# Performance work log

Hardware: AMD Instinct MI355X
Metric: run time of the kernel (lower is better)

Reference implementation:

```python
import jax, jax.numpy as jnp
import numpy as np

B, L, H = 2, 2048, 1024
NH, DK, DV = 4, 256, 256
CONV_K, FIR_S, FIR_L = 4, 3, 63
GATE_IN = H + 4 * 2 * NH  # 1056
MLP_H = 2 * H
CHUNK = 32


def l2norm(x):
    return x * jax.lax.rsqrt(jnp.sum(x * x, -1, keepdims=True) + 1e-6)


def causal_dwconv(x, w):
    # x: [b, l, c], w: [c, k]; causal depthwise cross-correlation == F.conv1d(pad left k-1, groups=c)
    k = w.shape[-1]
    xc = jnp.pad(jnp.transpose(x, (0, 2, 1)), ((0, 0), (0, 0), (k - 1, 0)))
    y = jax.lax.conv_general_dilated(xc, w[:, None, :], (1,), 'VALID',
                                     feature_group_count=w.shape[0],
                                     dimension_numbers=('NCH', 'OIH', 'NCH'))
    return jnp.transpose(y, (0, 2, 1))


def delta_rule_chunkwise(q, k, v, beta, chunk=CHUNK):
    # q,k: [b,h,L,dk]; v: [b,h,L,dv]; beta: [b,h,L]; L divisible by chunk
    b, h, Lp, dk = q.shape
    dv = v.shape[-1]
    n = Lp // chunk
    q = l2norm(q)
    k = l2norm(k)
    v = v * beta[..., None]
    kb = k * beta[..., None]
    qc, kc, vc, kbc = (t.reshape(b, h, n, chunk, -1) for t in (q, k, v, kb))
    # strictly-lower Gram matrix; the original in-place row loop computes inv(I + tril(kb k^T, -1))
    A = jnp.tril(jnp.einsum('bhnid,bhnjd->bhnij', kbc, kc), -1)
    T = jnp.linalg.inv(jnp.eye(chunk, dtype=q.dtype) + A)  # [b,h,n,c,c]
    u = T @ vc   # [b,h,n,c,dv]
    w = T @ kbc  # [b,h,n,c,dk]

    def step(S, inp):
        qi, ki, ui, wi = inp  # each [b,h,c,d]
        attn = jnp.tril(qi @ jnp.swapaxes(ki, -1, -2))  # keep diag (masked_fill triu(.,1))
        u2 = ui - wi @ S
        oi = qi @ S + attn @ u2
        return S + jnp.swapaxes(ki, -1, -2) @ u2, oi

    S0 = jnp.zeros((b, h, dk, dv), q.dtype)
    xs = tuple(jnp.moveaxis(t, 2, 0) for t in (qc, kc, u, w))
    S, o = jax.lax.scan(step, S0, xs)
    o = jnp.moveaxis(o, 0, 2).reshape(b, h, Lp, dv)
    return o, S


def branch_stats(x):
    # x: [b,l,h,d] -> [b,l,2h]  (mean and population-std, std clamped at sqrt(1e-6))
    m = x.mean(-1)
    s = jnp.sqrt(jnp.maximum(x.var(-1), 1e-6))
    return jnp.concatenate([m, s], -1)


def setup_inputs() -> dict:
    key = jax.random.key(0)
    ks = jax.random.split(key, 16)
    f32 = jnp.float32

    def dirac(k_, shape):
        f = 0.01 * jax.random.normal(k_, shape, f32)
        return f.at[..., shape[-1] // 2].add(1.0)

    b2 = jnp.zeros((NH * 4,), f32).at[jnp.arange(NH) * 4 + 3].set(2.0)
    return {
        'hidden_states': jax.random.normal(ks[0], (B, L, H), f32),
        'Wq': 0.02 * jax.random.normal(ks[1], (H, NH * DK), f32),
        'Wk': 0.02 * jax.random.normal(ks[2], (H, NH * DK), f32),
        'Wv': 0.02 * jax.random.normal(ks[3], (H, NH * DV), f32),
        'Wb': 0.02 * jax.random.normal(ks[4], (H, NH), f32),
        'conv_q_w': 0.2 * jax.random.normal(ks[5], (NH * DK, CONV_K), f32),
        'conv_k_w': 0.2 * jax.random.normal(ks[6], (NH * DK, CONV_K), f32),
        'conv_v_w': 0.2 * jax.random.normal(ks[7], (NH * DV, CONV_K), f32),
        'fir_short_w': dirac(ks[8], (NH, DV, FIR_S)),
        'fir_long_w': dirac(ks[9], (NH, DV, FIR_L)),
        'mlp_w1': 0.02 * jax.random.normal(ks[10], (GATE_IN, MLP_H), f32),
        'mlp_b1': jnp.zeros((MLP_H,), f32),
        'mlp_w2': 0.02 * jax.random.normal(ks[11], (MLP_H, NH * 4), f32),
        'mlp_b2': b2,
        'gate_log_temp': jnp.full((NH,), np.log(1.2), f32),
        'o_norm_w': jnp.ones((DV,), f32),
        'Wo': 0.02 * jax.random.normal(ks[12], (NH * DV, H), f32),
    }


def reference(hidden_states, Wq, Wk, Wv, Wb, conv_q_w, conv_k_w, conv_v_w,
              fir_short_w, fir_long_w, mlp_w1, mlp_b1, mlp_w2, mlp_b2,
              gate_log_temp, o_norm_w, Wo):
    x = hidden_states
    b, l, _ = x.shape
    # projections + short causal depthwise convs with silu (qk_activation='silu')
    q = jax.nn.silu(causal_dwconv(x @ Wq, conv_q_w)).reshape(b, l, NH, DK)
    k = jax.nn.silu(causal_dwconv(x @ Wk, conv_k_w)).reshape(b, l, NH, DK)
    v = jax.nn.silu(causal_dwconv(x @ Wv, conv_v_w)).reshape(b, l, NH, DV)
    beta = jax.nn.sigmoid(x @ Wb)  # [b,l,h]

    delta_out, _S = delta_rule_chunkwise(
        jnp.transpose(q, (0, 2, 1, 3)), jnp.transpose(k, (0, 2, 1, 3)),
        jnp.transpose(v, (0, 2, 1, 3)), jnp.transpose(beta, (0, 2, 1)))
    delta_out = jnp.transpose(delta_out, (0, 2, 1, 3))  # [b,l,h,dv]

    vf = v.reshape(b, l, NH * DV)
    fir_short = causal_dwconv(vf, fir_short_w.reshape(NH * DV, FIR_S)).reshape(b, l, NH, DV)
    fir_long = causal_dwconv(vf, fir_long_w.reshape(NH * DV, FIR_L)).reshape(b, l, NH, DV)

    gate_in = jnp.concatenate([x, branch_stats(fir_short), branch_stats(fir_long),
                               branch_stats(delta_out), branch_stats(v)], -1)
    logits = jax.nn.gelu(gate_in @ mlp_w1 + mlp_b1, approximate=False) @ mlp_w2 + mlp_b2
    temp = jax.nn.softplus(gate_log_temp) + 1e-4
    logits = logits.reshape(b, l, NH, 4) / temp[None, None, :, None]
    w = jax.nn.softmax(logits, -1)

    o = (w[..., 0:1] * fir_short + w[..., 1:2] * fir_long
         + w[..., 2:3] * delta_out + w[..., 3:4] * v)
    # RMSNorm over head_v_dim, eps=1e-5
    o = o * jax.lax.rsqrt(jnp.mean(o * o, -1, keepdims=True) + 1e-5) * o_norm_w
    return o.reshape(b, l, NH * DV) @ Wo
```

## Files before the change

### kernel.cpp

```cpp
#include <hip/hip_runtime.h>
#include <hip/hip_bf16.h>


#define DEVI __device__ __forceinline__
typedef unsigned int u32;
typedef unsigned short ushort_t;
typedef __attribute__((ext_vector_type(8))) short short8;
typedef __attribute__((ext_vector_type(4))) float floatx4;

constexpr int Ls = 2048, NH = 4;

constexpr size_t off_xq   = 0;
constexpr size_t off_xk   = 4194304;
constexpr size_t off_xv   = 8388608;
constexpr size_t off_q    = 12582912;
constexpr size_t off_k    = 16777216;
constexpr size_t off_v    = 20971520;
constexpr size_t off_beta = 25165824;
constexpr size_t off_attn = 25182208;
constexpr size_t off_firs = 25706496;
constexpr size_t off_firl = 29900800;
constexpr size_t off_gin  = 34095104;
constexpr size_t off_mlph = 38420480;
constexpr size_t off_gates= 46809088;

DEVI float sigmoidf_(float x) { return 1.f / (1.f + expf(-x)); }
DEVI float siluf_(float x) { return x / (1.f + expf(-x)); }
DEVI float geluf_(float x) { return 0.5f * x * (1.f + erff(x * 0.7071067811865476f)); }
DEVI ushort_t f2bf(float f) {
  union { float f; u32 u; } c{f};
  u32 r = (c.u + 0x7fffu + ((c.u >> 16) & 1u)) >> 16;
  return (ushort_t)r;
}
DEVI float bf2f(ushort_t h) {
  union { u32 u; float f; } c; c.u = ((u32)h) << 16; return c.f;
}
DEVI void cvt8(float4 a, float4 b, short8& hi, short8& lo) {
  float f[8] = {a.x,a.y,a.z,a.w,b.x,b.y,b.z,b.w};
#pragma unroll
  for (int j = 0; j < 8; ++j) {
    ushort_t h = f2bf(f[j]);
    hi[j] = (short)h;
    lo[j] = (short)f2bf(f[j] - bf2f(h));
  }
}
DEVI void async16(const void* g, void* l) {
  __builtin_amdgcn_global_load_lds(
      (const u32 __attribute__((address_space(1)))*)g,
      (u32 __attribute__((address_space(3)))*)l, 16, 0, 0);
}
DEVI void wave_barrier() {
  __builtin_amdgcn_sched_barrier(0);
  asm volatile("s_waitcnt lgkmcnt(0)" ::: "memory");
  __builtin_amdgcn_s_barrier();
  __builtin_amdgcn_sched_barrier(0);
}

__global__ __launch_bounds__(256) void to_bf16(
    const float* __restrict__ in, ushort_t* __restrict__ out, int n)
{
  int i = (blockIdx.x * 256 + threadIdx.x) * 8;
  if (i >= n) return;
  float4 a = *(const float4*)(in + i);
  float4 b = *(const float4*)(in + i + 4);
  ushort_t o[8] = { f2bf(a.x), f2bf(a.y), f2bf(a.z), f2bf(a.w),
                    f2bf(b.x), f2bf(b.y), f2bf(b.z), f2bf(b.w) };
  *(uint4*)(out + i) = *(uint4*)o;
}

__global__ __launch_bounds__(256) void convT(
    const float* __restrict__ W, ushort_t* __restrict__ out, int Kq, int Nq)
{
  __shared__ ushort_t tile[32][33];
  int n0 = blockIdx.x * 32, k0 = blockIdx.y * 32;
  int tx = threadIdx.x & 31, ty = threadIdx.x >> 5;
#pragma unroll
  for (int r = 0; r < 32; r += 8)
    tile[ty + r][tx] = f2bf(W[(size_t)(k0 + ty + r) * Nq + n0 + tx]);
  __syncthreads();
#pragma unroll
  for (int r = 0; r < 32; r += 8)
    out[(size_t)(n0 + ty + r) * Kq + k0 + tx] = tile[tx][ty + r];
}

__global__ __launch_bounds__(256) void gemm_bf16(
    const ushort_t* __restrict__ A, const ushort_t* __restrict__ Bt,
    float* __restrict__ C, int Nq, int Kq,
    const float* __restrict__ bias, int act, int outbf)
{
  __shared__ ushort_t As[128 * 32];
  __shared__ ushort_t Bs[128 * 32];
  int t = threadIdx.x;
  int w = t >> 6, lane = t & 63;
  int m0 = blockIdx.y * 128, n0 = blockIdx.x * 128;
  floatx4 acc[4][4];
#pragma unroll
  for (int i = 0; i < 4; ++i)
#pragma unroll
    for (int j = 0; j < 4; ++j)
#pragma unroll
      for (int r = 0; r < 4; ++r) acc[i][j][r] = 0.f;

  int lrow = lane >> 2, lk8 = (lane & 3) * 8;
  for (int kt = 0; kt < Kq; kt += 32) {
#pragma unroll
    for (int r = 0; r < 2; ++r) {
      int seg = w * 2 + r;
      int row = seg * 16 + lrow;
      async16(A  + (size_t)(m0 + row) * Kq + kt + lk8, &As[seg * 512]);
      async16(Bt + (size_t)(n0 + row) * Kq + kt + lk8, &Bs[seg * 512]);
    }
    __syncthreads();
    short8 af[4], bf[4];
#pragma unroll
    for (int i = 0; i < 4; ++i) {
      int row = (w >> 1) * 64 + i * 16 + (lane & 15);
      af[i] = *(const short8*)&As[row * 32 + (lane >> 4) * 8];
    }
#pragma unroll
    for (int j = 0; j < 4; ++j) {
      int col = (w & 1) * 64 + j * 16 + (lane & 15);
      bf[j] = *(const short8*)&Bs[col * 32 + (lane >> 4) * 8];
    }
#pragma unroll
    for (int i = 0; i < 4; ++i)
#pragma unroll
      for (int j = 0; j < 4; ++j)
        acc[i][j] = __builtin_amdgcn_mfma_f32_16x16x32_bf16(af[i], bf[j], acc[i][j], 0, 0, 0);
    __syncthreads();
  }
#pragma unroll
  for (int i = 0; i < 4; ++i) {
    int rbase = m0 + (w >> 1) * 64 + i * 16 + ((lane >> 4) << 2);
#pragma unroll
    for (int j = 0; j < 4; ++j) {
      int col = n0 + (w & 1) * 64 + j * 16 + (lane & 15);
      float bv = act ? bias[col] : 0.f;
#pragma unroll
      for (int r = 0; r < 4; ++r) {
        float v = acc[i][j][r];
        if (act) v = geluf_(v + bv);
        if (outbf) ((ushort_t*)C)[(size_t)(rbase + r) * Nq + col] = f2bf(v);
        else       C[(size_t)(rbase + r) * Nq + col] = v;
      }
    }
  }
}

__global__ __launch_bounds__(256) void beta_sigmoid(
    const float* __restrict__ x, const float* __restrict__ Wb,
    float* __restrict__ beta)
{
  int mtok = blockIdx.x, t = threadIdx.x;
  int b = mtok >> 11, l = mtok & 2047;
  float a0 = 0, a1 = 0, a2 = 0, a3 = 0;
  for (int k = t; k < 1024; k += 256) {
    float xv = x[(size_t)mtok * 1024 + k];
    float4 w4 = *(const float4*)(Wb + k * 4);
    a0 = fmaf(xv, w4.x, a0); a1 = fmaf(xv, w4.y, a1);
    a2 = fmaf(xv, w4.z, a2); a3 = fmaf(xv, w4.w, a3);
  }
#pragma unroll
  for (int off = 32; off; off >>= 1) {
    a0 += __shfl_down(a0, off); a1 += __shfl_down(a1, off);
    a2 += __shfl_down(a2, off); a3 += __shfl_down(a3, off);
  }
  __shared__ float red[4][4];
  int w = t >> 6;
  if ((t & 63) == 0) { red[w][0] = a0; red[w][1] = a1; red[w][2] = a2; red[w][3] = a3; }
  __syncthreads();
  if (t < 4) {
    float s = red[0][t] + red[1][t] + red[2][t] + red[3][t];
    beta[((size_t)(b * NH + t)) * Ls + l] = sigmoidf_(s);
  }
}

__global__ __launch_bounds__(256) void conv_prep(
    const float* __restrict__ x3, const float* __restrict__ wq,
    const float* __restrict__ wk, const float* __restrict__ wv,
    const float* __restrict__ beta_g,
    float* __restrict__ qn, float* __restrict__ kn,
    float* __restrict__ kb, float* __restrict__ vb,
    float* __restrict__ v_out)
{
  int i = blockIdx.x;
  int t = threadIdx.x;
  int l = i & 2047, bh = i >> 11;
  int b = bh >> 2, h = bh & 3;
  int c = h * 256 + t;
  const float* p = x3 + ((size_t)b * Ls) * 3072 + c;
  float4 wq4 = *(const float4*)(wq + c * 4);
  float4 wk4 = *(const float4*)(wk + c * 4);
  float4 wv4 = *(const float4*)(wv + c * 4);
  float qw[4] = {wq4.x, wq4.y, wq4.z, wq4.w};
  float kw[4] = {wk4.x, wk4.y, wk4.z, wk4.w};
  float vw[4] = {wv4.x, wv4.y, wv4.z, wv4.w};
  float aq = 0.f, ak = 0.f, av = 0.f;
#pragma unroll
  for (int j = 0; j < 4; ++j) {
    int ls = l - 3 + j;
    if (ls >= 0) {
      size_t rb = (size_t)ls * 3072;
      aq = fmaf(qw[j], p[rb], aq);
      ak = fmaf(kw[j], p[rb + 1024], ak);
      av = fmaf(vw[j], p[rb + 2048], av);
    }
  }
  float qv = siluf_(aq), kv = siluf_(ak), vv = siluf_(av);
  float sq = qv * qv, sk = kv * kv;
#pragma unroll
  for (int off = 32; off; off >>= 1) {
    sq += __shfl_down(sq, off);
    sk += __shfl_down(sk, off);
  }
  __shared__ float rq_[4], rk_[4];
  int w = t >> 6;
  if ((t & 63) == 0) { rq_[w] = sq; rk_[w] = sk; }
  __syncthreads();
  sq = rq_[0] + rq_[1] + rq_[2] + rq_[3];
  sk = rk_[0] + rk_[1] + rk_[2] + rk_[3];
  float rq = rsqrtf(sq + 1e-6f), rk = rsqrtf(sk + 1e-6f);
  float bt = beta_g[i];
  size_t base = (size_t)i * 256 + t;
  qn[base] = qv * rq;
  kn[base] = kv * rk;
  kb[base] = kv * rk * bt;
  vb[base] = vv * bt;
  v_out[base] = vv;
}

__global__ __launch_bounds__(256) void chunk_prep(
    const float* __restrict__ kb, const float* __restrict__ kn,
    const float* __restrict__ qn, const float* __restrict__ vb,
    float* __restrict__ attn_g, float* __restrict__ u_out,
    ushort_t* __restrict__ wn_bf, ushort_t* __restrict__ q_bf,
    ushort_t* __restrict__ knT_bf, ushort_t* __restrict__ kn_bf)
{
  __shared__ float Am[32][33];
  __shared__ float Tm[32][36];
  __shared__ ushort_t KT_hi[256][40];
  __shared__ ushort_t KT_lo[256][40];
  int t = threadIdx.x;
  int cc = blockIdx.x & 63, bh = blockIdx.x >> 6;
  size_t gbase = ((size_t)bh * Ls + cc * 32) * 256;
  int wv = t >> 6, lane = t & 63;
  int l16 = lane & 15, quad = lane >> 4;
  int mi = wv >> 1, ni = wv & 1;

  floatx4 Aacc = {0.f,0.f,0.f,0.f}, Qacc = {0.f,0.f,0.f,0.f};
  {
    int mrow = mi * 16 + l16, nrow = ni * 16 + l16;
    const float* kbp = kb + gbase + (size_t)mrow * 256;
    const float* qnp = qn + gbase + (size_t)mrow * 256;
    const float* knp = kn + gbase + (size_t)nrow * 256;
#pragma unroll
    for (int ks = 0; ks < 8; ++ks) {
      int koff = ks * 32 + quad * 8;
      short8 kbh, kbl, qnh, qnl, knh, knl;
      cvt8(*(const float4*)(kbp + koff), *(const float4*)(kbp + koff + 4), kbh, kbl);
      cvt8(*(const float4*)(qnp + koff), *(const float4*)(qnp + koff + 4), qnh, qnl);
      cvt8(*(const float4*)(knp + koff), *(const float4*)(knp + koff + 4), knh, knl);
      Aacc = __builtin_amdgcn_mfma_f32_16x16x32_bf16(kbh, knh, Aacc, 0, 0, 0);
      Aacc = __builtin_amdgcn_mfma_f32_16x16x32_bf16(kbh, knl, Aacc, 0, 0, 0);
      Aacc = __builtin_amdgcn_mfma_f32_16x16x32_bf16(kbl, knh, Aacc, 0, 0, 0);
      Qacc = __builtin_amdgcn_mfma_f32_16x16x32_bf16(qnh, knh, Qacc, 0, 0, 0);
      Qacc = __builtin_amdgcn_mfma_f32_16x16x32_bf16(qnh, knl, Qacc, 0, 0, 0);
      Qacc = __builtin_amdgcn_mfma_f32_16x16x32_bf16(qnl, knh, Qacc, 0, 0, 0);
      if (ni == 0)
        *(uint4*)(q_bf + gbase + (size_t)mrow * 256 + koff) = *(uint4*)&qnh;
      if (mi == 0)
        *(uint4*)(kn_bf + gbase + (size_t)nrow * 256 + koff) = *(uint4*)&knh;
    }
  }
  float* ag = attn_g + ((size_t)bh * 64 + cc) * 1024;
#pragma unroll
  for (int r = 0; r < 4; ++r) {
    int row = mi * 16 + quad * 4 + r, col = ni * 16 + l16;
    Am[row][col] = (col < row) ? Aacc[r] : 0.f;
    ag[row * 32 + col] = (col <= row) ? Qacc[r] : 0.f;
  }
  __syncthreads();

  if (wv == 0) {
    if (t < 32) {
#pragma unroll
      for (int i = 0; i < 32; ++i) Tm[i][t] = (i == t) ? 1.f : 0.f;
      for (int i2 = 1; i2 < 32; ++i2) {
        if (t < i2) {
          float s = 0.f;
          for (int m2 = t; m2 < i2; ++m2) s = fmaf(Am[i2][m2], Tm[m2][t], s);
          Tm[i2][t] = -s;
        }
      }
    }
  } else {
    int base = t - 64;
#pragma unroll
    for (int pass = 0; pass < 2; ++pass) {
      int d = base + pass * 192;
      if (d < 256) {
        u32 hp[16], lp[16], kp2[16];
#pragma unroll
        for (int m2 = 0; m2 < 16; ++m2) {
          float f0 = kb[gbase + (size_t)(2 * m2) * 256 + d];
          float f1 = kb[gbase + (size_t)(2 * m2 + 1) * 256 + d];
          ushort_t h0 = f2bf(f0), h1 = f2bf(f1);
          hp[m2] = (u32)h0 | ((u32)h1 << 16);
          lp[m2] = (u32)f2bf(f0 - bf2f(h0)) | ((u32)f2bf(f1 - bf2f(h1)) << 16);
          float g0 = kn[gbase + (size_t)(2 * m2) * 256 + d];
          float g1 = kn[gbase + (size_t)(2 * m2 + 1) * 256 + d];
          kp2[m2] = (u32)f2bf(g0) | ((u32)f2bf(g1) << 16);
        }
#pragma unroll
        for (int q2 = 0; q2 < 4; ++q2) {
          *(uint4*)&KT_hi[d][q2 * 8] = *(uint4*)&hp[q2 * 4];
          *(uint4*)&KT_lo[d][q2 * 8] = *(uint4*)&lp[q2 * 4];
          *(uint4*)(knT_bf + gbase + (size_t)d * 32 + q2 * 8) = *(uint4*)&kp2[q2 * 4];
        }
      }
    }
  }
  __syncthreads();

  int lt = wv & 1, dgrp = wv >> 1;
  short8 Th, Tl;
  {
    int lrow = lt * 16 + l16;
    cvt8(*(const float4*)&Tm[lrow][quad * 8],
         *(const float4*)&Tm[lrow][quad * 8 + 4], Th, Tl);
  }
#pragma unroll
  for (int j = 0; j < 8; ++j) {
    int dt = dgrp * 8 + j;
    short8 Bh = *(const short8*)&KT_hi[dt * 16 + l16][quad * 8];
    short8 Bl = *(const short8*)&KT_lo[dt * 16 + l16][quad * 8];
    floatx4 acc = {0.f,0.f,0.f,0.f};
    acc = __builtin_amdgcn_mfma_f32_16x16x32_bf16(Th, Bh, acc, 0, 0, 0);
    acc = __builtin_amdgcn_mfma_f32_16x16x32_bf16(Th, Bl, acc, 0, 0, 0);
    acc = __builtin_amdgcn_mfma_f32_16x16x32_bf16(Tl, Bh, acc, 0, 0, 0);
#pragma unroll
    for (int r = 0; r < 4; ++r) {
      int row = lt * 16 + quad * 4 + r;
      wn_bf[gbase + (size_t)row * 256 + dt * 16 + l16] = f2bf(-acc[r]);
    }
  }
  __syncthreads();

  {
    int d = t;
    u32 hp[16], lp[16];
#pragma unroll
    for (int m2 = 0; m2 < 16; ++m2) {
      float f0 = vb[gbase + (size_t)(2 * m2) * 256 + d];
      float f1 = vb[gbase + (size_t)(2 * m2 + 1) * 256 + d];
      ushort_t h0 = f2bf(f0), h1 = f2bf(f1);
      hp[m2] = (u32)h0 | ((u32)h1 << 16);
      lp[m2] = (u32)f2bf(f0 - bf2f(h0)) | ((u32)f2bf(f1 - bf2f(h1)) << 16);
    }
#pragma unroll
    for (int q2 = 0; q2 < 4; ++q2) {
      *(uint4*)&KT_hi[d][q2 * 8] = *(uint4*)&hp[q2 * 4];
      *(uint4*)&KT_lo[d][q2 * 8] = *(uint4*)&lp[q2 * 4];
    }
  }
  __syncthreads();

#pragma unroll
  for (int j = 0; j < 8; ++j) {
    int dt = dgrp * 8 + j;
    short8 Bh = *(const short8*)&KT_hi[dt * 16 + l16][quad * 8];
    short8 Bl = *(const short8*)&KT_lo[dt * 16 + l16][quad * 8];
    floatx4 acc = {0.f,0.f,0.f,0.f};
    acc = __builtin_amdgcn_mfma_f32_16x16x32_bf16(Th, Bh, acc, 0, 0, 0);
    acc = __builtin_amdgcn_mfma_f32_16x16x32_bf16(Th, Bl, acc, 0, 0, 0);
    acc = __builtin_amdgcn_mfma_f32_16x16x32_bf16(Tl, Bh, acc, 0, 0, 0);
#pragma unroll
    for (int r = 0; r < 4; ++r) {
      int row = lt * 16 + quad * 4 + r;
      u_out[gbase + (size_t)row * 256 + dt * 16 + l16] = acc[r];
    }
  }
}

__global__ __launch_bounds__(256) void cross_prep(
    const ushort_t* __restrict__ wn_bf, const ushort_t* __restrict__ q_bf,
    const ushort_t* __restrict__ kn_bf,
    float* __restrict__ X_g, float* __restrict__ Y_g)
{
  int t = threadIdx.x;
  int sc = blockIdx.x & 31, bh = blockIdx.x >> 5;
  int wv = t >> 6, lane = t & 63;
  int l16 = lane & 15, quad = lane >> 4;
  int mi = wv >> 1, ni = wv & 1;
  size_t base = (size_t)bh * Ls * 256;
  size_t r1 = base + (size_t)(sc * 64 + 32 + mi * 16 + l16) * 256;
  size_t r0 = base + (size_t)(sc * 64 + ni * 16 + l16) * 256;
  floatx4 Xacc = {0.f,0.f,0.f,0.f}, Yacc = {0.f,0.f,0.f,0.f};
#pragma unroll
  for (int ks = 0; ks < 8; ++ks) {
    int ko = ks * 32 + quad * 8;
    short8 aw = *(const short8*)(wn_bf + r1 + ko);
    short8 aq = *(const short8*)(q_bf  + r1 + ko);
    short8 bk = *(const short8*)(kn_bf + r0 + ko);
    Xacc = __builtin_amdgcn_mfma_f32_16x16x32_bf16(aw, bk, Xacc, 0, 0, 0);
    Yacc = __builtin_amdgcn_mfma_f32_16x16x32_bf16(aq, bk, Yacc, 0, 0, 0);
  }
  float* xo = X_g + ((size_t)bh * 32 + sc) * 1024;
  float* yo = Y_g + ((size_t)bh * 32 + sc) * 1024;
#pragma unroll
  for (int r = 0; r < 4; ++r) {
    int row = mi * 16 + quad * 4 + r, col = ni * 16 + l16;
    xo[row * 32 + col] = Xacc[r];
    yo[row * 32 + col] = Yacc[r];
  }
}

__global__ __launch_bounds__(256, 1) void delta_fir(
    const ushort_t* __restrict__ wn_bf, const ushort_t* __restrict__ q_bf,
    const ushort_t* __restrict__ knT_bf, const float* __restrict__ attn_g,
    const float* __restrict__ u_g, const float* __restrict__ X_g,
    const float* __restrict__ Y_g, float* __restrict__ delta_g,
    const float* __restrict__ v, const float* __restrict__ wlg,
    const float* __restrict__ wsg, float* __restrict__ firl,
    float* __restrict__ firs)
{
  __shared__ __attribute__((aligned(16))) char smem[72704];
  int t = threadIdx.x;

  if (blockIdx.x >= 128) {
    float (*vt)[71] = (float(*)[71])smem;
    int bid = blockIdx.x - 128;
    int lt = bid & 255;
    int bh = bid >> 8;
    int b = bh >> 2, h = bh & 3;
    int l0 = lt * 8;
    const float* vp = v + (size_t)bh * Ls * 256;
    for (int r = 0; r < 70; ++r) {
      int ls = l0 - 62 + r;
      vt[t][r] = (ls >= 0) ? vp[(size_t)ls * 256 + t] : 0.f;
    }
    float TL[63], TS3[3];
#pragma unroll
    for (int j = 0; j < 63; ++j) TL[j] = wlg[((size_t)h * 256 + t) * 63 + j];
#pragma unroll
    for (int j = 0; j < 3; ++j) TS3[j] = wsg[((size_t)h * 256 + t) * 3 + j];
    __syncthreads();
    float aL[8] = {0,0,0,0,0,0,0,0}, aS[8] = {0,0,0,0,0,0,0,0};
#pragma unroll
    for (int r = 0; r < 70; ++r) {
      float vm = vt[t][r];
#pragma unroll
      for (int p = 0; p < 8; ++p) {
        int jl = r - p;
        if (jl >= 0 && jl < 63) aL[p] = fmaf(vm, TL[jl], aL[p]);
        int jssrc = r - 60 - p;
        if (jssrc >= 0 && jssrc < 3) aS[p] = fmaf(vm, TS3[jssrc], aS[p]);
      }
    }
#pragma unroll
    for (int p = 0; p < 8; ++p) {
      int l = l0 + p;
      size_t ob = (((size_t)b * Ls + l) * NH + h) * 256 + t;
      firl[ob] = aL[p];
      firs[ob] = aS[p];
    }
    return;
  }

  ushort_t (*Shi)[264] = (ushort_t(*)[264])(smem);
  ushort_t (*Slo)[264] = (ushort_t(*)[264])(smem + 8448);
  float (*u2L0)[17] = (float(*)[17])(smem + 16896);
  float (*u2L1)[17] = (float(*)[17])(smem + 19072);
  int bh = blockIdx.x & 7, g = blockIdx.x >> 3;
  int b = bh >> 2, h = bh & 3;
  int wv = t >> 6, lane = t & 63;
  int lquad = lane >> 4, l16 = lane & 15;
  int j0 = g * 16;
  int Mt = wv & 1;
  bool isU = (wv < 2);
  const ushort_t* wp = wn_bf + (size_t)bh * Ls * 256;
  const ushort_t* qp = q_bf  + (size_t)bh * Ls * 256;
  const ushort_t* ap = (isU ? wp : qp) + (size_t)(Mt * 16 + l16) * 256;
  const ushort_t* kr = knT_bf + (size_t)bh * Ls * 256 + (size_t)l16 * 32 + lquad * 8;
  const float* urow = u_g + (size_t)bh * Ls * 256
                    + (size_t)(Mt * 16 + lquad * 4) * 256 + j0 + l16;
  const float* arp = attn_g + (size_t)bh * 64 * 1024
                   + (size_t)(Mt * 16 + l16) * 32 + lquad * 8;
  const float* xrp = (isU ? X_g : Y_g) + (size_t)bh * 32768
                   + (size_t)(Mt * 16 + l16) * 32 + lquad * 8;

  floatx4 Sacc[4], SaccL[4];
#pragma unroll
  for (int i = 0; i < 4; ++i)
#pragma unroll
    for (int r = 0; r < 4; ++r) { Sacc[i][r] = 0.f; SaccL[i][r] = 0.f; }
  for (int i = t; i < 4224; i += 256) ((u32*)smem)[i] = 0;

  short8 a0[8], k0[4];
  floatx4 u0 = {0.f, 0.f, 0.f, 0.f};
  float4 at0a = {0,0,0,0}, at0b = {0,0,0,0};
#pragma unroll
  for (int ks = 0; ks < 8; ++ks)
    a0[ks] = *(const short8*)(ap + ks * 32 + lquad * 8);
#pragma unroll
  for (int i = 0; i < 4; ++i)
    k0[i] = *(const short8*)(kr + (size_t)(wv * 4 + i) * 512);
  if (isU) {
#pragma unroll
    for (int r = 0; r < 4; ++r) u0[r] = urow[(size_t)r * 256];
  } else {
    at0a = *(const float4*)(arp);
    at0b = *(const float4*)(arp + 4);
  }
  wave_barrier();

  for (int sc = 0; sc < 32; ++sc) {
    size_t cb1 = (size_t)sc * 16384 + 8192;
    size_t nb0 = (size_t)(sc + 1) * 16384;
    bool hasN = (sc + 1 < 32);

    short8 a1[8], k1[4];
    floatx4 u1 = {0.f, 0.f, 0.f, 0.f};
    float4 at1a = {0,0,0,0}, at1b = {0,0,0,0};
#pragma unroll
    for (int ks = 0; ks < 8; ++ks)
      a1[ks] = *(const short8*)(ap + cb1 + ks * 32 + lquad * 8);
#pragma unroll
    for (int i = 0; i < 4; ++i)
      k1[i] = *(const short8*)(kr + cb1 + (size_t)(wv * 4 + i) * 512);
    if (isU) {
#pragma unroll
      for (int r = 0; r < 4; ++r) u1[r] = urow[cb1 + (size_t)r * 256];
    } else {
      size_t na = (size_t)(2 * sc + 1) * 1024;
      at1a = *(const float4*)(arp + na);
      at1b = *(const float4*)(arp + na + 4);
    }
    float4 xa = *(const float4*)(xrp + (size_t)sc * 1024);
    float4 xb = *(const float4*)(xrp + (size_t)sc * 1024 + 4);

    floatx4 acc0;
    if (isU) {
      floatx4 A0 = u0, A1 = {0,0,0,0}, A2 = {0,0,0,0}, A3 = {0,0,0,0};
#pragma unroll
      for (int ks = 0; ks < 8; ++ks) {
        short8 sh = *(const short8*)&Shi[l16][ks * 32 + lquad * 8];
        short8 sl = *(const short8*)&Slo[l16][ks * 32 + lquad * 8];
        if (ks & 1) {
          A1 = __builtin_amdgcn_mfma_f32_16x16x32_bf16(a0[ks], sh, A1, 0, 0, 0);
          A3 = __builtin_amdgcn_mfma_f32_16x16x32_bf16(a0[ks], sl, A3, 0, 0, 0);
        } else {
          A0 = __builtin_amdgcn_mfma_f32_16x16x32_bf16(a0[ks], sh, A0, 0, 0, 0);
          A2 = __builtin_amdgcn_mfma_f32_16x16x32_bf16(a0[ks], sl, A2, 0, 0, 0);
        }
      }
#pragma unroll
      for (int r = 0; r < 4; ++r) acc0[r] = (A0[r] + A1[r]) + (A2[r] + A3[r]);
#pragma unroll
      for (int r = 0; r < 4; ++r)
        u2L0[Mt * 16 + lquad * 4 + r][l16] = acc0[r];
    } else {
      floatx4 A0 = {0,0,0,0}, A1 = {0,0,0,0};
#pragma unroll
      for (int ks = 0; ks < 8; ++ks) {
        short8 sh = *(const short8*)&Shi[l16][ks * 32 + lquad * 8];
        if (ks & 1) A1 = __builtin_amdgcn_mfma_f32_16x16x32_bf16(a0[ks], sh, A1, 0, 0, 0);
        else        A0 = __builtin_amdgcn_mfma_f32_16x16x32_bf16(a0[ks], sh, A0, 0, 0, 0);
      }
#pragma unroll
      for (int r = 0; r < 4; ++r) acc0[r] = A0[r] + A1[r];
    }
    if (hasN) {
#pragma unroll
      for (int ks = 0; ks < 8; ++ks)
        a0[ks] = *(const short8*)(ap + nb0 + ks * 32 + lquad * 8);
    }
    wave_barrier();

    short8 uh0, ul0;
#pragma unroll
    for (int j = 0; j < 8; ++j) {
      float f = u2L0[lquad * 8 + j][l16];
      ushort_t hi = f2bf(f);
      uh0[j] = (short)hi;
      ul0[j] = (short)f2bf(f - bf2f(hi));
    }
#pragma unroll
    for (int i = 0; i < 4; ++i) {
      Sacc[i]  = __builtin_amdgcn_mfma_f32_16x16x32_bf16(k0[i], uh0, Sacc[i], 0, 0, 0);
      SaccL[i] = __builtin_amdgcn_mfma_f32_16x16x32_bf16(k0[i], ul0, SaccL[i], 0, 0, 0);
    }
    if (hasN) {
#pragma unroll
      for (int i = 0; i < 4; ++i)
        k0[i] = *(const short8*)(kr + nb0 + (size_t)(wv * 4 + i) * 512);
    }

    floatx4 acc1;
    if (isU) {
      floatx4 A0 = u1, A1 = {0,0,0,0}, A2 = {0,0,0,0}, A3 = {0,0,0,0};
#pragma unroll
      for (int ks = 0; ks < 8; ++ks) {
        short8 sh = *(const short8*)&Shi[l16][ks * 32 + lquad * 8];
        short8 sl = *(const short8*)&Slo[l16][ks * 32 + lquad * 8];
        if (ks & 1) {
          A1 = __builtin_amdgcn_mfma_f32_16x16x32_bf16(a1[ks], sh, A1, 0, 0, 0);
          A3 = __builtin_amdgcn_mfma_f32_16x16x32_bf16(a1[ks], sl, A3, 0, 0, 0);
        } else {
          A0 = __builtin_amdgcn_mfma_f32_16x16x32_bf16(a1[ks], sh, A0, 0, 0, 0);
          A2 = __builtin_amdgcn_mfma_f32_16x16x32_bf16(a1[ks], sl, A2, 0, 0, 0);
        }
      }
      short8 Xh, Xl;
      cvt8(xa, xb, Xh, Xl);
      A0 = __builtin_amdgcn_mfma_f32_16x16x32_bf16(Xh, uh0, A0, 0, 0, 0);
      A1 = __builtin_amdgcn_mfma_f32_16x16x32_bf16(Xh, ul0, A1, 0, 0, 0);
      A2 = __builtin_amdgcn_mfma_f32_16x16x32_bf16(Xl, uh0, A2, 0, 0, 0);
#pragma unroll
      for (int r = 0; r < 4; ++r) acc1[r] = (A0[r] + A1[r]) + (A2[r] + A3[r]);
#pragma unroll
      for (int r = 0; r < 4; ++r)
        u2L1[Mt * 16 + lquad * 4 + r][l16] = acc1[r];
      if (hasN) {
#pragma unroll
        for (int r = 0; r < 4; ++r) u0[r] = urow[nb0 + (size_t)r * 256];
      }
    } else {
      short8 ath, atl;
      cvt8(at0a, at0b, ath, atl);
      acc0 = __builtin_amdgcn_mfma_f32_16x16x32_bf16(ath, uh0, acc0, 0, 0, 0);
      acc0 = __builtin_amdgcn_mfma_f32_16x16x32_bf16(ath, ul0, acc0, 0, 0, 0);
      acc0 = __builtin_amdgcn_mfma_f32_16x16x32_bf16(atl, uh0, acc0, 0, 0, 0);
#pragma unroll
      for (int r = 0; r < 4; ++r) {
        int l = sc * 64 + Mt * 16 + lquad * 4 + r;
        delta_g[(((size_t)b * Ls + l) * NH + h) * 256 + j0 + l16] = acc0[r];
      }
      floatx4 A0 = {0,0,0,0}, A1 = {0,0,0,0};
#pragma unroll
      for (int ks = 0; ks < 8; ++ks) {
        short8 sh = *(const short8*)&Shi[l16][ks * 32 + lquad * 8];
        if (ks & 1) A1 = __builtin_amdgcn_mfma_f32_16x16x32_bf16(a1[ks], sh, A1, 0, 0, 0);
        else        A0 = __builtin_amdgcn_mfma_f32_16x16x32_bf16(a1[ks], sh, A0, 0, 0, 0);
      }
      short8 Yh, Yl;
      cvt8(xa, xb, Yh, Yl);
      A0 = __builtin_amdgcn_mfma_f32_16x16x32_bf16(Yh, uh0, A0, 0, 0, 0);
      A1 = __builtin_amdgcn_mfma_f32_16x16x32_bf16(Yh, ul0, A1, 0, 0, 0);
      A0 = __builtin_amdgcn_mfma_f32_16x16x32_bf16(Yl, uh0, A0, 0, 0, 0);
#pragma unroll
      for (int r = 0; r < 4; ++r) acc1[r] = A0[r] + A1[r];
      if (hasN) {
        size_t na0 = (size_t)(2 * sc + 2) * 1024;
        at0a = *(const float4*)(arp + na0);
        at0b = *(const float4*)(arp + na0 + 4);
      }
    }
    wave_barrier();

    short8 uh1, ul1;
#pragma unroll
    for (int j = 0; j < 8; ++j) {
      float f = u2L1[lquad * 8 + j][l16];
      ushort_t hi = f2bf(f);
      uh1[j] = (short)hi;
      ul1[j] = (short)f2bf(f - bf2f(hi));
    }
#pragma unroll
    for (int i = 0; i < 4; ++i) {
      Sacc[i]  = __builtin_amdgcn_mfma_f32_16x16x32_bf16(k1[i], uh1, Sacc[i], 0, 0, 0);
      SaccL[i] = __builtin_amdgcn_mfma_f32_16x16x32_bf16(k1[i], ul1, SaccL[i], 0, 0, 0);
    }
    if (!isU) {
      short8 ath, atl;
      cvt8(at1a, at1b, ath, atl);
      acc1 = __builtin_amdgcn_mfma_f32_16x16x32_bf16(ath, uh1, acc1, 0, 0, 0);
      acc1 = __builtin_amdgcn_mfma_f32_16x16x32_bf16(ath, ul1, acc1, 0, 0, 0);
      acc1 = __builtin_amdgcn_mfma_f32_16x16x32_bf16(atl, uh1, acc1, 0, 0, 0);
#pragma unroll
      for (int r = 0; r < 4; ++r) {
        int l = sc * 64 + 32 + Mt * 16 + lquad * 4 + r;
        delta_g[(((size_t)b * Ls + l) * NH + h) * 256 + j0 + l16] = acc1[r];
      }
    }
#pragma unroll
    for (int i = 0; i < 4; ++i) {
      int dk0 = (wv * 4 + i) * 16 + lquad * 4;
      ushort4 h4, l4;
      ushort_t* hp = (ushort_t*)&h4;
      ushort_t* lp = (ushort_t*)&l4;
#pragma unroll
      for (int r = 0; r < 4; ++r) {
        float sv = Sacc[i][r] + SaccL[i][r];
        ushort_t hi = f2bf(sv);
        hp[r] = hi;
        lp[r] = f2bf(sv - bf2f(hi));
      }
      *(ushort4*)&Shi[l16][dk0] = h4;
      *(ushort4*)&Slo[l16][dk0] = l4;
    }
    wave_barrier();
  }
}

__global__ __launch_bounds__(256) void build_gate_in_bf(
    const float* __restrict__ x, const float* __restrict__ firs,
    const float* __restrict__ firl, const float* __restrict__ delta,
    const float* __restrict__ v, ushort_t* __restrict__ gin)
{
  int mtok = blockIdx.x, t = threadIdx.x;
  int b = mtok >> 11, l = mtok & 2047;
  float4 xv = *(const float4*)(x + (size_t)mtok * 1024 + t * 4);
  ushort4 xo = make_ushort4(f2bf(xv.x), f2bf(xv.y), f2bf(xv.z), f2bf(xv.w));
  *(ushort4*)(gin + (size_t)mtok * 1056 + t * 4) = xo;
  int w = t >> 6, lane = t & 63;
  for (int br = 0; br < 4; ++br) {
    float s = 0.f, s2 = 0.f;
#pragma unroll
    for (int r = 0; r < 4; ++r) {
      int d = lane + r * 64;
      float val;
      if (br == 0)      val = firs [(size_t)mtok * 1024 + w * 256 + d];
      else if (br == 1) val = firl [(size_t)mtok * 1024 + w * 256 + d];
      else if (br == 2) val = delta[(size_t)mtok * 1024 + w * 256 + d];
      else              val = v[(((size_t)(b * NH + w)) * Ls + l) * 256 + d];
      s += val; s2 = fmaf(val, val, s2);
    }
#pragma unroll
    for (int off = 32; off; off >>= 1) {
      s += __shfl_down(s, off);
      s2 += __shfl_down(s2, off);
    }
    if (lane == 0) {
      float mean = s * (1.f / 256.f);
      float var = s2 * (1.f / 256.f) - mean * mean;
      gin[(size_t)mtok * 1056 + 1024 + br * 8 + w] = f2bf(mean);
      gin[(size_t)mtok * 1056 + 1024 + br * 8 + 4 + w] = f2bf(sqrtf(fmaxf(var, 1e-6f)));
    }
  }
}

__global__ __launch_bounds__(256) void mlp2_gates(
    const ushort_t* __restrict__ mh, const float* __restrict__ W2,
    const float* __restrict__ b2, const float* __restrict__ glt,
    float* __restrict__ gates)
{
  int mtok = blockIdx.x, t = threadIdx.x;
  float p[16];
#pragma unroll
  for (int j = 0; j < 16; ++j) p[j] = 0.f;
  for (int k = t; k < 2048; k += 256) {
    float hv = bf2f(mh[(size_t)mtok * 2048 + k]);
    const float* wr = W2 + (size_t)k * 16;
#pragma unroll
    for (int j4 = 0; j4 < 4; ++j4) {
      float4 w4 = *(const float4*)(wr + j4 * 4);
      p[j4*4+0] = fmaf(hv, w4.x, p[j4*4+0]);
      p[j4*4+1] = fmaf(hv, w4.y, p[j4*4+1]);
      p[j4*4+2] = fmaf(hv, w4.z, p[j4*4+2]);
      p[j4*4+3] = fmaf(hv, w4.w, p[j4*4+3]);
    }
  }
#pragma unroll
  for (int j = 0; j < 16; ++j)
#pragma unroll
    for (int off = 32; off; off >>= 1) p[j] += __shfl_down(p[j], off);
  __shared__ float red[4][16];
  __shared__ float zl[16];
  int w = t >> 6;
  if ((t & 63) == 0) {
#pragma unroll
    for (int j = 0; j < 16; ++j) red[w][j] = p[j];
  }
  __syncthreads();
  if (t < 16) {
    float tot = red[0][t] + red[1][t] + red[2][t] + red[3][t] + b2[t];
    float tempv = log1pf(expf(glt[t >> 2])) + 1e-4f;
    zl[t] = tot / tempv;
  }
  __syncthreads();
  if (t < 4) {
    float z0 = zl[t*4], z1 = zl[t*4+1], z2 = zl[t*4+2], z3 = zl[t*4+3];
    float mx = fmaxf(fmaxf(z0, z1), fmaxf(z2, z3));
    float e0 = expf(z0 - mx), e1 = expf(z1 - mx), e2 = expf(z2 - mx), e3 = expf(z3 - mx);
    float inv = 1.f / (e0 + e1 + e2 + e3);
    gates[(size_t)mtok * 16 + t * 4 + 0] = e0 * inv;
    gates[(size_t)mtok * 16 + t * 4 + 1] = e1 * inv;
    gates[(size_t)mtok * 16 + t * 4 + 2] = e2 * inv;
    gates[(size_t)mtok * 16 + t * 4 + 3] = e3 * inv;
  }
}

__global__ __launch_bounds__(256) void combine_norm_bf(
    const float* __restrict__ firs, const float* __restrict__ firl,
    const float* __restrict__ delta, const float* __restrict__ v,
    const float* __restrict__ gates, const float* __restrict__ onw,
    ushort_t* __restrict__ o)
{
  int mh = blockIdx.x;
  int mtok = mh >> 2, h = mh & 3;
  int t = threadIdx.x;
  int b = mtok >> 11, l = mtok & 2047;
  const float* g = gates + (size_t)mtok * 16 + h * 4;
  float w0 = g[0], w1 = g[1], w2 = g[2], w3 = g[3];
  size_t tb = (size_t)mtok * 1024 + h * 256 + t;
  float val = w0 * firs[tb] + w1 * firl[tb] + w2 * delta[tb]
            + w3 * v[(((size_t)(b * NH + h)) * Ls + l) * 256 + t];
  float s2 = val * val;
#pragma unroll
  for (int off = 32; off; off >>= 1) s2 += __shfl_down(s2, off);
  __shared__ float r4[4];
  if ((t & 63) == 0) r4[t >> 6] = s2;
  __syncthreads();
  float tot = r4[0] + r4[1] + r4[2] + r4[3];
  float rms = rsqrtf(tot * (1.f / 256.f) + 1e-5f);
  o[tb] = f2bf(val * rms * onw[t]);
}

extern "C" void kernel_launch(void* const* d_in, const int* in_sizes, int n_in,
                              void* d_out, int out_size, void* d_ws, size_t ws_size,
                              hipStream_t stream) {
  const float* x     = (const float*)d_in[0];
  const float* Wq    = (const float*)d_in[1];
  const float* Wk    = (const float*)d_in[2];
  const float* Wv    = (const float*)d_in[3];
  const float* Wb    = (const float*)d_in[4];
  const float* convq = (const float*)d_in[5];
  const float* convk = (const float*)d_in[6];
  const float* convv = (const float*)d_in[7];
  const float* firsw = (const float*)d_in[8];
  const float* firlw = (const float*)d_in[9];
  const float* mlpw1 = (const float*)d_in[10];
  const float* mlpb1 = (const float*)d_in[11];
  const float* mlpw2 = (const float*)d_in[12];
  const float* mlpb2 = (const float*)d_in[13];
  const float* glt   = (const float*)d_in[14];
  const float* onw   = (const float*)d_in[15];
  const float* Wo    = (const float*)d_in[16];
  float* ws = (float*)d_ws;

  ushort_t* x_bf   = (ushort_t*)(ws + off_firs);
  ushort_t* Wqkv_t = (ushort_t*)(ws + off_firl);
  ushort_t* gin_bf = (ushort_t*)(ws + off_gin);
  ushort_t* w1_t   = (ushort_t*)(ws + off_k);
  ushort_t* o_bf   = (ushort_t*)(ws + off_xv);
  ushort_t* Wo_t   = (ushort_t*)(ws + off_beta);
  ushort_t* mlph_bf= (ushort_t*)(ws + off_mlph);
  ushort_t* wn_bf  = (ushort_t*)(ws + off_firs);
  ushort_t* q_bf   = (ushort_t*)(ws + off_firs + 2097152);
  ushort_t* knT_bf = (ushort_t*)(ws + off_firl);
  ushort_t* kn_bf  = (ushort_t*)(ws + off_xq);
  float* x3   = ws + off_xq;
  float* kb_f = ws + off_gin;
  float* vb_f = ws + off_mlph;
  float* X_g  = ws + off_gin;
  float* Y_g  = ws + off_gin + 262144;
  float* firs_f = ws + off_xq;
  float* firl_f = ws + off_xk;

  dim3 blk(256);
  to_bf16<<<2048, blk, 0, stream>>>(x, x_bf, 4194304);
  convT<<<dim3(32, 32), blk, 0, stream>>>(Wq, Wqkv_t, 1024, 1024);
  convT<<<dim3(32, 32), blk, 0, stream>>>(Wk, Wqkv_t + 1048576, 1024, 1024);
  convT<<<dim3(32, 32), blk, 0, stream>>>(Wv, Wqkv_t + 2097152, 1024, 1024);
  gemm_bf16<<<dim3(24, 32), blk, 0, stream>>>(x_bf, Wqkv_t, x3, 3072, 1024, nullptr, 0, 0);
  beta_sigmoid<<<4096, blk, 0, stream>>>(x, Wb, ws + off_beta);
  conv_prep<<<16384, blk, 0, stream>>>(x3, convq, convk, convv, ws + off_beta,
                                       ws + off_q, ws + off_k, kb_f, vb_f, ws + off_v);
  chunk_prep<<<512, blk, 0, stream>>>(kb_f, ws + off_k, ws + off_q, vb_f,
                                      ws + off_attn, ws + off_xv, wn_bf, q_bf,
                                      knT_bf, kn_bf);
  cross_prep<<<256, blk, 0, stream>>>(wn_bf, q_bf, kn_bf, X_g, Y_g);
  delta_fir<<<2176, blk, 0, stream>>>(wn_bf, q_bf, knT_bf, ws + off_attn,
                                      ws + off_xv, X_g, Y_g, ws + off_q,
                                      ws + off_v, firlw, firsw, firl_f, firs_f);
  build_gate_in_bf<<<4096, blk, 0, stream>>>(x, firs_f, firl_f, ws + off_q,
                                             ws + off_v, gin_bf);
  convT<<<dim3(64, 33), blk, 0, stream>>>(mlpw1, w1_t, 1056, 2048);
  gemm_bf16<<<dim3(16, 32), blk, 0, stream>>>(gin_bf, w1_t, (float*)mlph_bf,
                                              2048, 1056, mlpb1, 1, 1);
  mlp2_gates<<<4096, blk, 0, stream>>>(mlph_bf, mlpw2, mlpb2, glt, ws + off_gates);
  combine_norm_bf<<<16384, blk, 0, stream>>>(firs_f, firl_f, ws + off_q,
                                             ws + off_v, ws + off_gates, onw, o_bf);
  convT<<<dim3(32, 32), blk, 0, stream>>>(Wo, Wo_t, 1024, 1024);
  gemm_bf16<<<dim3(8, 32), blk, 0, stream>>>(o_bf, Wo_t, (float*)d_out, 1024, 1024, nullptr, 0, 0);
}
```

Before: 545.6 us.

## Pack two work units per 512-thread block in delta_fir kernel

Doubles the block size of the fused delta-rule/FIR kernel to 512 threads, with each half of the block running an independent work unit (a delta-rule column slice or a FIR tile) in its own shared-memory region. The FIR halves cover adjacent time tiles and share one widened staged window of v, which cuts redundant halo loads. The launch bound changes from (256,1) to (512,2), which squeezes the register budget for the 63-tap FIR path and the MFMA accumulators and risks spilling. Any wave-level barriers in the delta path must still be correct for the half-block split.

```diff
diff --git a/kernel.cpp b/kernel.cpp
--- a/kernel.cpp
+++ b/kernel.cpp
@@ -415,7 +415,7 @@
   }
 }
 
-__global__ __launch_bounds__(256, 1) void delta_fir(
+__global__ __launch_bounds__(512, 2) void delta_fir(
     const ushort_t* __restrict__ wn_bf, const ushort_t* __restrict__ q_bf,
     const ushort_t* __restrict__ knT_bf, const float* __restrict__ attn_g,
     const float* __restrict__ u_g, const float* __restrict__ X_g,
@@ -424,31 +424,35 @@
     const float* __restrict__ wsg, float* __restrict__ firl,
     float* __restrict__ firs)
 {
-  __shared__ __attribute__((aligned(16))) char smem[72704];
+  __shared__ __attribute__((aligned(16))) char smem[81920];
   int t = threadIdx.x;
 
-  if (blockIdx.x >= 128) {
-    float (*vt)[71] = (float(*)[71])smem;
-    int bid = blockIdx.x - 128;
-    int lt = bid & 255;
-    int bh = bid >> 8;
+  if (blockIdx.x >= 64) {
+    float (*vt)[79] = (float(*)[79])smem;
+    int bid = blockIdx.x - 64;
+    int half = t >> 8, c = t & 255;
+    int unit = bid * 2 + half;
+    int lt = unit & 255;
+    int bh = unit >> 8;
     int b = bh >> 2, h = bh & 3;
     int l0 = lt * 8;
+    int base_l = ((bid * 2) & 255) * 8 - 62;
     const float* vp = v + (size_t)bh * Ls * 256;
+    for (int r = half * 39; r < half * 39 + 39 && r < 78; ++r) {
+      int ls = base_l + r;
+      vt[c][r] = (ls >= 0) ? vp[(size_t)ls * 256 + c] : 0.f;
+    }
+    float TL[63], TS3[3];
+#pragma unroll
+    for (int j = 0; j < 63; ++j) TL[j] = wlg[((size_t)h * 256 + c) * 63 + j];
+#pragma unroll
+    for (int j = 0; j < 3; ++j) TS3[j] = wsg[((size_t)h * 256 + c) * 3 + j];
+    __syncthreads();
+    int roff = half * 8;
+    float aL[8] = {0,0,0,0,0,0,0,0}, aS[8] = {0,0,0,0,0,0,0,0};
+#pragma unroll
     for (int r = 0; r < 70; ++r) {
-      int ls = l0 - 62 + r;
-      vt[t][r] = (ls >= 0) ? vp[(size_t)ls * 256 + t] : 0.f;
-    }
-    float TL[63], TS3[3];
-#pragma unroll
-    for (int j = 0; j < 63; ++j) TL[j] = wlg[((size_t)h * 256 + t) * 63 + j];
-#pragma unroll
-    for (int j = 0; j < 3; ++j) TS3[j] = wsg[((size_t)h * 256 + t) * 3 + j];
-    __syncthreads();
-    float aL[8] = {0,0,0,0,0,0,0,0}, aS[8] = {0,0,0,0,0,0,0,0};
-#pragma unroll
-    for (int r = 0; r < 70; ++r) {
-      float vm = vt[t][r];
+      float vm = vt[c][roff + r];
 #pragma unroll
       for (int p = 0; p < 8; ++p) {
         int jl = r - p;
@@ -460,20 +464,23 @@
 #pragma unroll
     for (int p = 0; p < 8; ++p) {
       int l = l0 + p;
-      size_t ob = (((size_t)b * Ls + l) * NH + h) * 256 + t;
+      size_t ob = (((size_t)b * Ls + l) * NH + h) * 256 + c;
       firl[ob] = aL[p];
       firs[ob] = aS[p];
     }
     return;
   }
 
-  ushort_t (*Shi)[264] = (ushort_t(*)[264])(smem);
-  ushort_t (*Slo)[264] = (ushort_t(*)[264])(smem + 8448);
-  float (*u2L0)[17] = (float(*)[17])(smem + 16896);
-  float (*u2L1)[17] = (float(*)[17])(smem + 19072);
-  int bh = blockIdx.x & 7, g = blockIdx.x >> 3;
+  int half = t >> 8, tt = t & 255;
+  char* cbase = smem + half * 21248;
+  ushort_t (*Shi)[264] = (ushort_t(*)[264])(cbase);
+  ushort_t (*Slo)[264] = (ushort_t(*)[264])(cbase + 8448);
+  float (*u2L0)[17] = (float(*)[17])(cbase + 16896);
+  float (*u2L1)[17] = (float(*)[17])(cbase + 19072);
+  int unit = blockIdx.x * 2 + half;
+  int bh = unit & 7, g = unit >> 3;
   int b = bh >> 2, h = bh & 3;
-  int wv = t >> 6, lane = t & 63;
+  int wv = tt >> 6, lane = tt & 63;
   int lquad = lane >> 4, l16 = lane & 15;
   int j0 = g * 16;
   int Mt = wv & 1;
@@ -494,7 +501,7 @@
   for (int i = 0; i < 4; ++i)
 #pragma unroll
     for (int r = 0; r < 4; ++r) { Sacc[i][r] = 0.f; SaccL[i][r] = 0.f; }
-  for (int i = t; i < 4224; i += 256) ((u32*)smem)[i] = 0;
+  for (int i = tt; i < 4224; i += 256) ((u32*)cbase)[i] = 0;
 
   short8 a0[8], k0[4];
   floatx4 u0 = {0.f, 0.f, 0.f, 0.f};
@@ -871,9 +878,9 @@
                                       ws + off_attn, ws + off_xv, wn_bf, q_bf,
                                       knT_bf, kn_bf);
   cross_prep<<<256, blk, 0, stream>>>(wn_bf, q_bf, kn_bf, X_g, Y_g);
-  delta_fir<<<2176, blk, 0, stream>>>(wn_bf, q_bf, knT_bf, ws + off_attn,
-                                      ws + off_xv, X_g, Y_g, ws + off_q,
-                                      ws + off_v, firlw, firsw, firl_f, firs_f);
+  delta_fir<<<1088, dim3(512), 0, stream>>>(wn_bf, q_bf, knT_bf, ws + off_attn,
+                                            ws + off_xv, X_g, Y_g, ws + off_q,
+                                            ws + off_v, firlw, firsw, firl_f, firs_f);
   build_gate_in_bf<<<4096, blk, 0, stream>>>(x, firs_f, firl_f, ws + off_q,
                                              ws + off_v, gin_bf);
   convT<<<dim3(64, 33), blk, 0, stream>>>(mlpw1, w1_t, 1056, 2048);
```

Result: slower. 632.2 us (+15.9%).
